# Optimization experiments

Measured on AMD Instinct MI355X. Metric: run time of the kernel, lower is better.

## Reference

```python
import jax, jax.numpy as jnp
import numpy as np
from functools import partial

LEAK = 1.0 / 3.0   # scn default leakiness 0.333
EPS = 1e-4         # scn BatchNormalization default eps


def linkey(c, S):
    return (c[..., 0] * S + c[..., 1]) * S + c[..., 2]


def sub_offsets(K):
    r = K // 2
    g = np.stack(np.meshgrid(*([np.arange(-r, r + 1)] * 3), indexing='ij'), -1).reshape(-1, 3)
    return jnp.asarray(g, jnp.int32)


def down_offsets(s):
    g = np.stack(np.meshgrid(*([np.arange(s)] * 3), indexing='ij'), -1).reshape(-1, 3)
    return jnp.asarray(g, jnp.int32)


@partial(jax.checkpoint, static_argnums=(4, 5))
def sparse_conv(out_coords, in_coords, in_feats, W, S_in, stride, offsets):
    """Rulebook gather-GEMM-scatter via sorted-key binary search.
    out_coords [M,3], in_coords [N,3] sorted by linearized key, in_feats [N,Cin],
    W [K3,Cin,Cout]. Submanifold: stride=1, centered offsets, out_coords==in_coords.
    Strided scn.Convolution: offsets 0..stride-1, out sites = unique(in//stride)."""
    in_keys = linkey(in_coords, S_in)  # sorted [N]
    Nin = in_keys.shape[0]

    def body(acc, kw):
        off, Wk = kw
        child = out_coords * stride + off                       # [M,3]
        valid = jnp.all((child >= 0) & (child < S_in), axis=-1)
        nkey = linkey(child, S_in)
        idx = jnp.searchsorted(in_keys, nkey)
        idxc = jnp.clip(idx, 0, Nin - 1)
        found = valid & (in_keys[idxc] == nkey)
        g = jnp.where(found[:, None], in_feats[idxc], 0.0)      # gather, zero for inactive
        return acc + g @ Wk, None

    acc0 = jnp.zeros((out_coords.shape[0], W.shape[-1]), in_feats.dtype)
    acc, _ = jax.lax.scan(body, acc0, (offsets, W))
    return acc


def bn_lrelu(x, g, b):
    m = x.mean(0)
    v = x.var(0)
    y = (x - m) * (g / jnp.sqrt(v + EPS)) + b
    return jnp.where(y > 0, y, LEAK * y)


def lrelu(x):
    return jnp.where(x > 0, x, LEAK * x)


def forward_core(floats, c0, c1, c2, c3, c4):
    (feats0, W_init, Wd1, gd1, bd1, W11a, g11, b11, W11b,
     W12a, g12, b12, W12b, Wd2, gd2, bd2,
     W21a, g21, b21, W21b, W22a, g22, b22, W22b,
     Wd3, gd3, bd3, Wd4, gd4, bd4, W2, b2, W3, b3) = floats
    o3 = sub_offsets(3)
    x = sparse_conv(c0, c0, feats0, W_init, 512, 1, sub_offsets(7))                 # [N0,64] @512
    x = bn_lrelu(sparse_conv(c1, c0, x, Wd1, 512, 2, down_offsets(2)), gd1, bd1)    # [N1,64] @256
    res = x
    h = bn_lrelu(sparse_conv(c1, c1, x, W11a, 256, 1, o3), g11, b11)
    x = lrelu(sparse_conv(c1, c1, h, W11b, 256, 1, o3) + res)
    res = x
    h = bn_lrelu(sparse_conv(c1, c1, x, W12a, 256, 1, o3), g12, b12)
    x = lrelu(sparse_conv(c1, c1, h, W12b, 256, 1, o3) + res)
    x = bn_lrelu(sparse_conv(c2, c1, x, Wd2, 256, 2, down_offsets(2)), gd2, bd2)    # [N2,128] @128
    res = x
    h = bn_lrelu(sparse_conv(c2, c2, x, W21a, 128, 1, o3), g21, b21)
    x = lrelu(sparse_conv(c2, c2, h, W21b, 128, 1, o3) + res)
    res = x
    h = bn_lrelu(sparse_conv(c2, c2, x, W22a, 128, 1, o3), g22, b22)
    x = lrelu(sparse_conv(c2, c2, h, W22b, 128, 1, o3) + res)
    x = bn_lrelu(sparse_conv(c3, c2, x, Wd3, 128, 4, down_offsets(4)), gd3, bd3)    # [N3,64] @32
    x = bn_lrelu(sparse_conv(c4, c3, x, Wd4, 32, 4, down_offsets(4)), gd4, bd4)     # [N4,2]  @8
    # SparseToDense -> dense [2,8,8,8], then torch .view(-1, 2*8*8*8) (channel-major)
    k4 = linkey(c4, 8)
    dense = jnp.zeros((8 * 8 * 8, 2), x.dtype).at[k4].set(x)    # [512,2]
    flat = dense.T.reshape(1, -1)                               # [1,1024]
    v = jax.nn.elu(flat @ W2 + b2)
    return jax.nn.sigmoid(v @ W3 + b3)                          # [1,1]


def _decode(k, S):
    a = k // (S * S)
    r = k % (S * S)
    return np.stack([a, r // S, r % S], -1).astype(np.int32)


def setup_inputs() -> dict:
    rng = np.random.default_rng(0)
    N0 = 50000
    k0 = np.unique(rng.integers(0, 512 ** 3, size=N0 + 20000))[:N0]
    c0 = _decode(k0, 512)
    c1 = _decode(np.unique((c0[:, 0].astype(np.int64) // 2 * 256 + c0[:, 1] // 2) * 256 + c0[:, 2] // 2), 256)
    c2 = _decode(np.unique((c1[:, 0].astype(np.int64) // 2 * 128 + c1[:, 1] // 2) * 128 + c1[:, 2] // 2), 128)
    c3 = _decode(np.unique((c2[:, 0].astype(np.int64) // 4 * 32 + c2[:, 1] // 4) * 32 + c2[:, 2] // 4), 32)
    c4 = _decode(np.unique((c3[:, 0].astype(np.int64) // 4 * 8 + c3[:, 1] // 4) * 8 + c3[:, 2] // 4), 8)
    key = jax.random.key(0)
    ks = jax.random.split(key, 20)

    def w(i, shape, fan):
        return jax.random.normal(ks[i], shape, jnp.float32) / np.float32(np.sqrt(fan))

    return dict(
        feats0=jax.random.normal(ks[0], (N0, 1), jnp.float32),
        W_init=w(1, (343, 1, 64), 343.0),
        Wd1=w(2, (8, 64, 64), 8 * 64), gd1=jnp.ones(64), bd1=jnp.zeros(64),
        W11a=w(3, (27, 64, 64), 27 * 64), g11=jnp.ones(64), b11=jnp.zeros(64),
        W11b=w(4, (27, 64, 64), 27 * 64),
        W12a=w(5, (27, 64, 64), 27 * 64), g12=jnp.ones(64), b12=jnp.zeros(64),
        W12b=w(6, (27, 64, 64), 27 * 64),
        Wd2=w(7, (8, 64, 128), 8 * 64), gd2=jnp.ones(128), bd2=jnp.zeros(128),
        W21a=w(8, (27, 128, 128), 27 * 128), g21=jnp.ones(128), b21=jnp.zeros(128),
        W21b=w(9, (27, 128, 128), 27 * 128),
        W22a=w(10, (27, 128, 128), 27 * 128), g22=jnp.ones(128), b22=jnp.zeros(128),
        W22b=w(11, (27, 128, 128), 27 * 128),
        Wd3=w(12, (64, 128, 64), 64 * 128), gd3=jnp.ones(64), bd3=jnp.zeros(64),
        Wd4=w(13, (64, 64, 2), 64 * 64), gd4=jnp.ones(2), bd4=jnp.zeros(2),
        W2=w(14, (1024, 2), 1024.0), b2=jnp.zeros(2),
        W3=w(15, (2, 1), 2.0), b3=jnp.zeros(1),
        coords0=jnp.asarray(c0), coords1=jnp.asarray(c1), coords2=jnp.asarray(c2),
        coords3=jnp.asarray(c3), coords4=jnp.asarray(c4),
    )


def reference(feats0, W_init, Wd1, gd1, bd1, W11a, g11, b11, W11b, W12a, g12, b12, W12b,
              Wd2, gd2, bd2, W21a, g21, b21, W21b, W22a, g22, b22, W22b,
              Wd3, gd3, bd3, Wd4, gd4, bd4, W2, b2, W3, b3,
              coords0, coords1, coords2, coords3, coords4):
    floats = (feats0, W_init, Wd1, gd1, bd1, W11a, g11, b11, W11b, W12a, g12, b12, W12b,
              Wd2, gd2, bd2, W21a, g21, b21, W21b, W22a, g22, b22, W22b,
              Wd3, gd3, bd3, Wd4, gd4, bd4, W2, b2, W3, b3)
    return forward_core(floats, coords0, coords1, coords2, coords3, coords4)
```

## Files before the change

kernel.cpp:

```cpp
#include <hip/hip_runtime.h>

#define LEAKF (1.0f/3.0f)
#define BN_EPS 1e-4f

__device__ __forceinline__ unsigned hmix(int key) {
    unsigned h = (unsigned)key * 2654435761u;
    h ^= h >> 15;
    return h;
}

__device__ __forceinline__ int hlookup(const int* __restrict__ hk,
                                       const int* __restrict__ hv,
                                       int mask, int key) {
    unsigned h = hmix(key) & (unsigned)mask;
    while (true) {
        int k = hk[h];
        if (k == key) return hv[h];
        if (k == -1) return -1;
        h = (h + 1) & (unsigned)mask;
    }
}

__device__ __forceinline__ float bnl(float v, float s, float h) {
    v = v * s + h;
    return v > 0.f ? v : v * LEAKF;
}

__global__ __launch_bounds__(256) void build_hash_bm_all(
    int B0, int B1, int B2,
    int N0, const int* __restrict__ c0, int* __restrict__ hk0, int* __restrict__ hv0,
    int m0, unsigned* __restrict__ bm0,
    int N1, const int* __restrict__ c1, int* __restrict__ hk1, int* __restrict__ hv1,
    int m1, unsigned* __restrict__ bm1,
    int N2, const int* __restrict__ c2, int* __restrict__ hk2, int* __restrict__ hv2,
    int m2, unsigned* __restrict__ bm2,
    int N3, const int* __restrict__ c3, int* __restrict__ hk3, int* __restrict__ hv3,
    int m3) {
    const int* coords; int* hk; int* hv; unsigned* bm; int mask, S, N, i;
    int b = blockIdx.x;
    if (b < B0)           { coords = c0; hk = hk0; hv = hv0; bm = bm0; mask = m0; S = 512; N = N0; i = b * 256 + threadIdx.x; }
    else if (b < B0 + B1) { coords = c1; hk = hk1; hv = hv1; bm = bm1; mask = m1; S = 256; N = N1; i = (b - B0) * 256 + threadIdx.x; }
    else if (b < B0 + B1 + B2) { coords = c2; hk = hk2; hv = hv2; bm = bm2; mask = m2; S = 128; N = N2; i = (b - B0 - B1) * 256 + threadIdx.x; }
    else                  { coords = c3; hk = hk3; hv = hv3; bm = nullptr; mask = m3; S = 32; N = N3; i = (b - B0 - B1 - B2) * 256 + threadIdx.x; }
    if (i >= N) return;
    int key = (coords[3 * i] * S + coords[3 * i + 1]) * S + coords[3 * i + 2];
    if (bm) atomicOr(&bm[key >> 5], 1u << (key & 31));
    unsigned h = hmix(key) & (unsigned)mask;
    while (true) {
        int old = atomicCAS(&hk[h], -1, key);
        if (old == -1 || old == key) { hv[h] = i; break; }
        h = (h + 1) & (unsigned)mask;
    }
}

__global__ __launch_bounds__(256) void rb_sub_bm(
    int B1,
    int N1, const int* __restrict__ c1, const unsigned* __restrict__ bm1,
    const int* __restrict__ hk1, const int* __restrict__ hv1, int m1,
    int2* __restrict__ rb1, int* __restrict__ cnt1, int cap1,
    int N2, const int* __restrict__ c2, const unsigned* __restrict__ bm2,
    const int* __restrict__ hk2, const int* __restrict__ hv2, int m2,
    int2* __restrict__ rb2, int* __restrict__ cnt2, int cap2) {
    __shared__ int lcnt[27];
    __shared__ int lbase[27];
    int tid = threadIdx.x;
    if (tid < 27) lcnt[tid] = 0;
    __syncthreads();
    const int* coords; const unsigned* bm; const int* hk; const int* hv;
    int mask, S, N, t; int2* pairs; int* counts; int cap;
    if (blockIdx.x < B1) {
        coords = c1; bm = bm1; hk = hk1; hv = hv1; mask = m1; S = 256; N = N1;
        pairs = rb1; counts = cnt1; cap = cap1; t = blockIdx.x * 256 + tid;
    } else {
        coords = c2; bm = bm2; hk = hk2; hv = hv2; mask = m2; S = 128; N = N2;
        pairs = rb2; counts = cnt2; cap = cap2; t = (blockIdx.x - B1) * 256 + tid;
    }
    unsigned bits = 0;
    int m = 0, kmin = 0, z = 0, dx = 0, dy = 0;
    int rk[3], ix[3];
    if (t < N * 9) {
        m = t / 9;
        int od = t - m * 9;
        dx = od / 3 - 1;
        dy = od - (od / 3) * 3 - 1;
        int x = coords[3 * m] + dx;
        int y = coords[3 * m + 1] + dy;
        z = coords[3 * m + 2];
        if ((unsigned)x < (unsigned)S && (unsigned)y < (unsigned)S) {
            int zmin = z - 1 < 0 ? 0 : z - 1;
            int zmax = z + 1 > S - 1 ? S - 1 : z + 1;
            kmin = (x * S + y) * S + zmin;
            int wi = kmin >> 5, sh = kmin & 31, nb = zmax - zmin + 1;
            unsigned long long w =
                ((unsigned long long)bm[wi + 1] << 32) | (unsigned long long)bm[wi];
            bits = (unsigned)((w >> sh) & ((1u << nb) - 1u));
            if (dx == 0 && dy == 0) bits &= ~(1u << (z - zmin));
            unsigned tmp = bits;
            int nf = 0;
            while (tmp) {
                int bb = __ffs(tmp) - 1;
                tmp &= tmp - 1;
                ix[nf] = hlookup(hk, hv, mask, kmin + bb);
                int dz = (kmin & (S - 1)) + bb - z;
                int k = (dx + 1) * 9 + (dy + 1) * 3 + (dz + 1);
                rk[nf] = atomicAdd(&lcnt[k], 1);
                nf++;
            }
        }
    }
    __syncthreads();
    if (tid < 27 && lcnt[tid] > 0) lbase[tid] = atomicAdd(&counts[tid], lcnt[tid]);
    __syncthreads();
    {
        unsigned tmp = bits;
        int j = 0;
        while (tmp) {
            int bb = __ffs(tmp) - 1;
            tmp &= tmp - 1;
            int dz = (kmin & (S - 1)) + bb - z;
            int k = (dx + 1) * 9 + (dy + 1) * 3 + (dz + 1);
            int p = lbase[k] + rk[j];
            if (p < cap) pairs[(size_t)k * cap + p] = make_int2(m, ix[j]);
            j++;
        }
    }
}

__global__ __launch_bounds__(256) void rb_down_all(
    int B1, int B2,
    int N0, const int* __restrict__ c0, const int* __restrict__ hk1,
    const int* __restrict__ hv1, int m1, int2* __restrict__ rbD1,
    int* __restrict__ cntD1, int capD1,
    int N1, const int* __restrict__ c1, const int* __restrict__ hk2,
    const int* __restrict__ hv2, int m2, int2* __restrict__ rbD2,
    int* __restrict__ cntD2, int capD2,
    int N2, const int* __restrict__ c2, const int* __restrict__ hk3,
    const int* __restrict__ hv3, int m3, int2* __restrict__ rbD3,
    int* __restrict__ cntD3, int capD3) {
    __shared__ int lcnt[64];
    __shared__ int lbase[64];
    int tid = threadIdx.x;
    const int* cin; const int* hk; const int* hv;
    int mask, Sout, s, Nin, i; int2* pairs; int* counts; int cap;
    int b = blockIdx.x;
    if (b < B1) {
        cin = c0; hk = hk1; hv = hv1; mask = m1; Sout = 256; s = 2; Nin = N0;
        pairs = rbD1; counts = cntD1; cap = capD1; i = b * 256 + tid;
    } else if (b < B1 + B2) {
        cin = c1; hk = hk2; hv = hv2; mask = m2; Sout = 128; s = 2; Nin = N1;
        pairs = rbD2; counts = cntD2; cap = capD2; i = (b - B1) * 256 + tid;
    } else {
        cin = c2; hk = hk3; hv = hv3; mask = m3; Sout = 32; s = 4; Nin = N2;
        pairs = rbD3; counts = cntD3; cap = capD3; i = (b - B1 - B2) * 256 + tid;
    }
    int K3 = s * s * s;
    if (tid < K3) lcnt[tid] = 0;
    __syncthreads();
    int k = -1, m = -1, rank = 0;
    if (i < Nin) {
        int x = cin[3 * i], y = cin[3 * i + 1], z = cin[3 * i + 2];
        k = ((x % s) * s + (y % s)) * s + (z % s);
        int key = ((x / s) * Sout + (y / s)) * Sout + (z / s);
        m = hlookup(hk, hv, mask, key);
        rank = atomicAdd(&lcnt[k], 1);
    }
    __syncthreads();
    if (tid < K3 && lcnt[tid] > 0) lbase[tid] = atomicAdd(&counts[tid], lcnt[tid]);
    __syncthreads();
    if (i < Nin) {
        int p = lbase[k] + rank;
        if (p < cap) pairs[(size_t)k * cap + p] = make_int2(m, i);
    }
}

__global__ __launch_bounds__(256) void init_probe(
    int total, int chunk, const int* __restrict__ c0, const unsigned* __restrict__ bm,
    const int* __restrict__ hk, const int* __restrict__ hv, int mask,
    int2* __restrict__ pairs, int* __restrict__ pcount, int cap) {
    __shared__ int lcnt, lbase;
    int tid = threadIdx.x;
    if (tid == 0) lcnt = 0;
    __syncthreads();
    int b = blockIdx.x;
    int nb = (b & 7) * chunk + (b >> 3);
    int t = nb * 256 + tid;
    unsigned bits = 0;
    int m = -1, kmin = 0, z = 0, dx = 0, dy = 0, rank = 0;
    if (t < total) {
        m = t / 49;
        int od = t - m * 49;
        dx = od / 7 - 3;
        dy = od - (od / 7) * 7 - 3;
        int x = c0[3 * m] + dx;
        int y = c0[3 * m + 1] + dy;
        z = c0[3 * m + 2];
        if ((unsigned)x < 512u && (unsigned)y < 512u) {
            int zmin = z - 3 < 0 ? 0 : z - 3;
            int zmax = z + 3 > 511 ? 511 : z + 3;
            kmin = (x * 512 + y) * 512 + zmin;
            int wi = kmin >> 5, sh = kmin & 31, nb2 = zmax - zmin + 1;
            unsigned long long w =
                ((unsigned long long)bm[wi + 1] << 32) | (unsigned long long)bm[wi];
            bits = (unsigned)((w >> sh) & ((1u << nb2) - 1u));
            if (dx == 0 && dy == 0) bits &= ~(1u << (z - zmin));
            if (bits) rank = atomicAdd(&lcnt, __popc(bits));
        }
    }
    __syncthreads();
    if (tid == 0 && lcnt > 0) lbase = atomicAdd(pcount, lcnt);
    __syncthreads();
    while (bits) {
        int b2 = __ffs(bits) - 1;
        bits &= bits - 1;
        int nkey = kmin + b2;
        int idx = hlookup(hk, hv, mask, nkey);
        int dz = (kmin & 511) + b2 - z;
        int k = (dx + 3) * 49 + (dy + 3) * 7 + (dz + 3);
        int p = lbase + rank++;
        if (p < cap) pairs[p] = make_int2(m, idx | (k << 17));
    }
}

__global__ __launch_bounds__(256) void init_center(
    int N0, const float* __restrict__ f0, const float* __restrict__ W,
    float* __restrict__ out) {
    int t = blockIdx.x * 256 + threadIdx.x;
    if (t >= N0 * 64) return;
    int m = t >> 6, co = t & 63;
    out[t] = f0[m] * W[171 * 64 + co];
}

__global__ __launch_bounds__(256) void init_apply(
    const int2* __restrict__ pairs, const int* __restrict__ pcount, int cap,
    const float* __restrict__ f0, const float* __restrict__ W,
    float* __restrict__ out) {
    int P = min(*pcount, cap);
    int t = blockIdx.x * 256 + threadIdx.x;
    if (t >= P * 64) return;
    int p = t >> 6, co = t & 63;
    int2 pr = pairs[p];
    int idx = pr.y & 0x1FFFF, k = pr.y >> 17;
    atomicAdd(&out[(size_t)pr.x * 64 + co], f0[idx] * W[k * 64 + co]);
}

template <int C, int TS, bool BNF>
__global__ __launch_bounds__(256) void center_gemm(
    int N, const float* __restrict__ inF, const float* __restrict__ Wc,
    float* __restrict__ out, const float* __restrict__ scp,
    const float* __restrict__ shp) {
    constexpr int C4 = C / 4;
    constexpr int SP = TS / 8;
    __shared__ float sW[C * 64];
    __shared__ float4 sRow[TS * C4];
    int tid = threadIdx.x;
    int t0 = blockIdx.x * TS;
    int co0 = blockIdx.y << 6;
    for (int e = tid; e < C * 16; e += 256) {
        int ci = e >> 4, c4 = e & 15;
        ((float4*)sW)[e] = *(const float4*)(Wc + (size_t)ci * C + co0 + c4 * 4);
    }
    for (int e = tid; e < TS * C4; e += 256) {
        int p = e / C4, c4 = e - p * C4;
        float4 v = make_float4(0.f, 0.f, 0.f, 0.f);
        if (t0 + p < N) {
            v = ((const float4*)inF)[(size_t)(t0 + p) * C4 + c4];
            if (BNF) {
                float4 s4 = ((const float4*)scp)[c4];
                float4 h4 = ((const float4*)shp)[c4];
                v.x = bnl(v.x, s4.x, h4.x);
                v.y = bnl(v.y, s4.y, h4.y);
                v.z = bnl(v.z, s4.z, h4.z);
                v.w = bnl(v.w, s4.w, h4.w);
            }
        }
        sRow[e] = v;
    }
    __syncthreads();
    int co = tid & 31, sg = tid >> 5;
    float accA[SP], accB[SP];
#pragma unroll
    for (int j = 0; j < SP; j++) { accA[j] = 0.f; accB[j] = 0.f; }
    for (int c4 = 0; c4 < C4; c4++) {
        float a0 = sW[(c4 * 4 + 0) * 64 + co];
        float a1 = sW[(c4 * 4 + 1) * 64 + co];
        float a2 = sW[(c4 * 4 + 2) * 64 + co];
        float a3 = sW[(c4 * 4 + 3) * 64 + co];
        float b0 = sW[(c4 * 4 + 0) * 64 + co + 32];
        float b1 = sW[(c4 * 4 + 1) * 64 + co + 32];
        float b2 = sW[(c4 * 4 + 2) * 64 + co + 32];
        float b3 = sW[(c4 * 4 + 3) * 64 + co + 32];
#pragma unroll
        for (int j = 0; j < SP; j++) {
            float4 r = sRow[(sg * SP + j) * C4 + c4];
            accA[j] += r.x * a0 + r.y * a1 + r.z * a2 + r.w * a3;
            accB[j] += r.x * b0 + r.y * b1 + r.z * b2 + r.w * b3;
        }
    }
#pragma unroll
    for (int j = 0; j < SP; j++) {
        int p = sg * SP + j;
        if (t0 + p < N) {
            out[(size_t)(t0 + p) * C + co0 + co] = accA[j];
            out[(size_t)(t0 + p) * C + co0 + co + 32] = accB[j];
        }
    }
}

template <int CIN, int P, int MODE>
__global__ __launch_bounds__(256) void pair_gemm(
    const float* __restrict__ inF, const float* __restrict__ inF2,
    const float* __restrict__ W, float* __restrict__ out,
    const int2* __restrict__ pairs, const int* __restrict__ counts,
    int cap, int chunksPerK, int COUT,
    const float* __restrict__ scp, const float* __restrict__ shp) {
    constexpr int C4 = CIN / 4;
    constexpr int SP = P / 8;
    __shared__ float sW[CIN * 64];
    __shared__ float4 sRow[P * C4];
    __shared__ int sM[P];
    __shared__ int sIdx[P];
    int k = blockIdx.x / chunksPerK;
    int chunk = blockIdx.x - k * chunksPerK;
    int cnt = min(counts[k], cap);
    int base = chunk * P;
    if (base >= cnt) return;
    int Pact = min(P, cnt - base);
    int tid = threadIdx.x;
    if (tid < P) {
        if (tid < Pact) {
            int2 pr = pairs[(size_t)k * cap + base + tid];
            sM[tid] = pr.x;
            sIdx[tid] = pr.y;
        } else {
            sM[tid] = -1;
            sIdx[tid] = 0;
        }
    }
    __syncthreads();
    int co0 = blockIdx.y << 6;
    const float* gW = W + (size_t)k * CIN * COUT + co0;
    for (int e = tid; e < CIN * 16; e += 256) {
        int ci = e >> 4, c4 = e & 15;
        ((float4*)sW)[e] = *(const float4*)(gW + (size_t)ci * COUT + c4 * 4);
    }
    for (int e = tid; e < P * C4; e += 256) {
        int p = e / C4, c4 = e - p * C4;
        float4 v = make_float4(0.f, 0.f, 0.f, 0.f);
        if (p < Pact) {
            v = ((const float4*)inF)[(size_t)sIdx[p] * C4 + c4];
            if (MODE == 1) {
                float4 s4 = ((const float4*)scp)[c4];
                float4 h4 = ((const float4*)shp)[c4];
                v.x = bnl(v.x, s4.x, h4.x);
                v.y = bnl(v.y, s4.y, h4.y);
                v.z = bnl(v.z, s4.z, h4.z);
                v.w = bnl(v.w, s4.w, h4.w);
            } else if (MODE == 2) {
                float4 u = ((const float4*)inF2)[(size_t)sIdx[p] * C4 + c4];
                v.x += u.x; v.y += u.y; v.z += u.z; v.w += u.w;
                v.x = v.x > 0.f ? v.x : v.x * LEAKF;
                v.y = v.y > 0.f ? v.y : v.y * LEAKF;
                v.z = v.z > 0.f ? v.z : v.z * LEAKF;
                v.w = v.w > 0.f ? v.w : v.w * LEAKF;
            }
        }
        sRow[e] = v;
    }
    __syncthreads();
    int co = tid & 31, sg = tid >> 5;
    float accA[SP], accB[SP];
#pragma unroll
    for (int j = 0; j < SP; j++) { accA[j] = 0.f; accB[j] = 0.f; }
    for (int c4 = 0; c4 < C4; c4++) {
        float a0 = sW[(c4 * 4 + 0) * 64 + co];
        float a1 = sW[(c4 * 4 + 1) * 64 + co];
        float a2 = sW[(c4 * 4 + 2) * 64 + co];
        float a3 = sW[(c4 * 4 + 3) * 64 + co];
        float b0 = sW[(c4 * 4 + 0) * 64 + co + 32];
        float b1 = sW[(c4 * 4 + 1) * 64 + co + 32];
        float b2 = sW[(c4 * 4 + 2) * 64 + co + 32];
        float b3 = sW[(c4 * 4 + 3) * 64 + co + 32];
#pragma unroll
        for (int j = 0; j < SP; j++) {
            float4 r = sRow[(sg * SP + j) * C4 + c4];
            accA[j] += r.x * a0 + r.y * a1 + r.z * a2 + r.w * a3;
            accB[j] += r.x * b0 + r.y * b1 + r.z * b2 + r.w * b3;
        }
    }
#pragma unroll
    for (int j = 0; j < SP; j++) {
        int p = sg * SP + j;
        if (p < Pact) {
            atomicAdd(&out[(size_t)sM[p] * COUT + co0 + co], accA[j]);
            atomicAdd(&out[(size_t)sM[p] * COUT + co0 + co + 32], accB[j]);
        }
    }
}

__global__ __launch_bounds__(64) void convd4_kernel(
    int M, const int* __restrict__ oc, const float* __restrict__ x3,
    const float* __restrict__ W, float* __restrict__ out4,
    const int* __restrict__ hk, const int* __restrict__ hv, int mask,
    const float* __restrict__ scp, const float* __restrict__ shp) {
    __shared__ int sIdx[64];
    __shared__ int sK[64];
    __shared__ int sCount;
    int m = blockIdx.x, tid = threadIdx.x;
    int cx = oc[3 * m], cy = oc[3 * m + 1], cz = oc[3 * m + 2];
    if (tid == 0) sCount = 0;
    __syncthreads();
    {
        int k = tid;
        int a = k >> 4, b = (k >> 2) & 3, c = k & 3;
        int x = cx * 4 + a, y = cy * 4 + b, z = cz * 4 + c;
        int key = (x * 32 + y) * 32 + z;
        int idx = hlookup(hk, hv, mask, key);
        if (idx >= 0) { int p = atomicAdd(&sCount, 1); sIdx[p] = idx; sK[p] = k; }
    }
    __syncthreads();
    int cnt = sCount;
    float s = scp[tid], h = shp[tid];
    float a0 = 0.f, a1 = 0.f;
    for (int j = 0; j < cnt; j++) {
        int idx = sIdx[j], k = sK[j];
        float f = bnl(x3[(size_t)idx * 64 + tid], s, h);
        const float* wk = W + ((size_t)k * 64 + tid) * 2;
        a0 += f * wk[0];
        a1 += f * wk[1];
    }
    for (int o = 32; o > 0; o >>= 1) {
        a0 += __shfl_down(a0, o);
        a1 += __shfl_down(a1, o);
    }
    if (tid == 0) { out4[2 * m] = a0; out4[2 * m + 1] = a1; }
}

__global__ __launch_bounds__(256) void bn_reduce_fin(
    const float4* __restrict__ X4, int total4, int B4, int C, int Cmask, float invN,
    const float* __restrict__ g, const float* __restrict__ b,
    float* __restrict__ sums, int* __restrict__ done,
    float* __restrict__ sc, float* __restrict__ sh) {
    __shared__ float sS[128];
    __shared__ float sQ[128];
    __shared__ int isLast;
    int tid = threadIdx.x;
    if (tid < C) { sS[tid] = 0.f; sQ[tid] = 0.f; }
    __syncthreads();
    int base4 = blockIdx.x * B4;
    int end4 = min(base4 + B4, total4);
    float s0 = 0.f, s1 = 0.f, s2 = 0.f, s3 = 0.f;
    float q0 = 0.f, q1 = 0.f, q2 = 0.f, q3 = 0.f;
    for (int e4 = base4 + tid; e4 < end4; e4 += 256) {
        float4 v = X4[e4];
        s0 += v.x; q0 += v.x * v.x;
        s1 += v.y; q1 += v.y * v.y;
        s2 += v.z; q2 += v.z * v.z;
        s3 += v.w; q3 += v.w * v.w;
    }
    int c0 = (4 * (base4 + tid)) & Cmask;
    atomicAdd(&sS[c0], s0);               atomicAdd(&sQ[c0], q0);
    atomicAdd(&sS[(c0 + 1) & Cmask], s1); atomicAdd(&sQ[(c0 + 1) & Cmask], q1);
    atomicAdd(&sS[(c0 + 2) & Cmask], s2); atomicAdd(&sQ[(c0 + 2) & Cmask], q2);
    atomicAdd(&sS[(c0 + 3) & Cmask], s3); atomicAdd(&sQ[(c0 + 3) & Cmask], q3);
    __syncthreads();
    if (tid < C) {
        atomicAdd(&sums[tid], sS[tid]);
        atomicAdd(&sums[128 + tid], sQ[tid]);
    }
    __syncthreads();
    if (tid == 0) {
        __threadfence();
        int t = atomicAdd(done, 1);
        isLast = (t == (int)gridDim.x - 1);
    }
    __syncthreads();
    if (isLast) {
        if (tid < C) {
            float v1 = atomicAdd(&sums[tid], 0.0f);
            float v2 = atomicAdd(&sums[128 + tid], 0.0f);
            float mean = v1 * invN;
            float var = v2 * invN - mean * mean;
            float s = g[tid] / sqrtf(var + BN_EPS);
            sc[tid] = s;
            sh[tid] = b[tid] - mean * s;
            sums[tid] = 0.f;
            sums[128 + tid] = 0.f;
        }
        if (tid == 0) *done = 0;
    }
}

__global__ __launch_bounds__(256) void add_lrelu_bn(const float4* __restrict__ A,
                                                    const float4* __restrict__ X,
                                                    float4* __restrict__ Y, int total4,
                                                    int C4mask,
                                                    const float* __restrict__ scp,
                                                    const float* __restrict__ shp) {
    int e = blockIdx.x * 256 + threadIdx.x;
    if (e >= total4) return;
    int c4 = e & C4mask;
    float4 s4 = ((const float4*)scp)[c4];
    float4 h4 = ((const float4*)shp)[c4];
    float4 a = A[e], x = X[e], v;
    v.x = a.x + bnl(x.x, s4.x, h4.x);
    v.y = a.y + bnl(x.y, s4.y, h4.y);
    v.z = a.z + bnl(x.z, s4.z, h4.z);
    v.w = a.w + bnl(x.w, s4.w, h4.w);
    v.x = v.x > 0.f ? v.x : v.x * LEAKF;
    v.y = v.y > 0.f ? v.y : v.y * LEAKF;
    v.z = v.z > 0.f ? v.z : v.z * LEAKF;
    v.w = v.w > 0.f ? v.w : v.w * LEAKF;
    Y[e] = v;
}

__global__ __launch_bounds__(256) void bn_scatter(int M, const int* __restrict__ c4,
                                                  const float* __restrict__ x4,
                                                  const float* __restrict__ sc,
                                                  const float* __restrict__ sh,
                                                  float* __restrict__ dense) {
    int i = blockIdx.x * 256 + threadIdx.x;
    if (i >= 2 * M) return;
    int m = i >> 1, co = i & 1;
    float v = x4[i] * sc[co] + sh[co];
    v = v > 0.f ? v : v * LEAKF;
    int key = (c4[3 * m] * 8 + c4[3 * m + 1]) * 8 + c4[3 * m + 2];
    dense[key * 2 + co] = v;
}

__global__ __launch_bounds__(256) void head_kernel(const float* __restrict__ dense,
                                                   const float* __restrict__ W2,
                                                   const float* __restrict__ b2,
                                                   const float* __restrict__ W3,
                                                   const float* __restrict__ b3,
                                                   float* __restrict__ out) {
    __shared__ float r0[256];
    __shared__ float r1[256];
    int tid = threadIdx.x;
    float a0 = 0.f, a1 = 0.f;
    for (int j = tid; j < 1024; j += 256) {
        int co = j >> 9, k = j & 511;
        float f = dense[k * 2 + co];
        a0 += f * W2[2 * j];
        a1 += f * W2[2 * j + 1];
    }
    r0[tid] = a0;
    r1[tid] = a1;
    __syncthreads();
    for (int s = 128; s > 0; s >>= 1) {
        if (tid < s) { r0[tid] += r0[tid + s]; r1[tid] += r1[tid + s]; }
        __syncthreads();
    }
    if (tid == 0) {
        float v0 = r0[0] + b2[0];
        float v1 = r1[0] + b2[1];
        v0 = v0 > 0.f ? v0 : expm1f(v0);
        v1 = v1 > 0.f ? v1 : expm1f(v1);
        float z = v0 * W3[0] + v1 * W3[1] + b3[0];
        out[0] = 1.f / (1.f + expf(-z));
    }
}

extern "C" void kernel_launch(void* const* d_in, const int* in_sizes, int n_in,
                              void* d_out, int out_size, void* d_ws, size_t ws_size,
                              hipStream_t stream) {
    const float* F0    = (const float*)d_in[0];
    const float* Winit = (const float*)d_in[1];
    const float* Wd1   = (const float*)d_in[2];
    const float* gd1   = (const float*)d_in[3];
    const float* bd1   = (const float*)d_in[4];
    const float* W11a  = (const float*)d_in[5];
    const float* g11   = (const float*)d_in[6];
    const float* b11   = (const float*)d_in[7];
    const float* W11b  = (const float*)d_in[8];
    const float* W12a  = (const float*)d_in[9];
    const float* g12   = (const float*)d_in[10];
    const float* b12   = (const float*)d_in[11];
    const float* W12b  = (const float*)d_in[12];
    const float* Wd2   = (const float*)d_in[13];
    const float* gd2   = (const float*)d_in[14];
    const float* bd2   = (const float*)d_in[15];
    const float* W21a  = (const float*)d_in[16];
    const float* g21   = (const float*)d_in[17];
    const float* b21   = (const float*)d_in[18];
    const float* W21b  = (const float*)d_in[19];
    const float* W22a  = (const float*)d_in[20];
    const float* g22   = (const float*)d_in[21];
    const float* b22   = (const float*)d_in[22];
    const float* W22b  = (const float*)d_in[23];
    const float* Wd3   = (const float*)d_in[24];
    const float* gd3   = (const float*)d_in[25];
    const float* bd3   = (const float*)d_in[26];
    const float* Wd4   = (const float*)d_in[27];
    const float* gd4   = (const float*)d_in[28];
    const float* bd4   = (const float*)d_in[29];
    const float* W2    = (const float*)d_in[30];
    const float* b2    = (const float*)d_in[31];
    const float* W3    = (const float*)d_in[32];
    const float* b3    = (const float*)d_in[33];
    const int* c0 = (const int*)d_in[34];
    const int* c1 = (const int*)d_in[35];
    const int* c2 = (const int*)d_in[36];
    const int* c3 = (const int*)d_in[37];
    const int* c4 = (const int*)d_in[38];
    int N0 = in_sizes[34] / 3, N1 = in_sizes[35] / 3, N2 = in_sizes[36] / 3;
    int N3 = in_sizes[37] / 3, N4 = in_sizes[38] / 3;

    char* base = (char*)d_ws;
    size_t off = 0;
    auto alloc = [&](size_t bytes) -> void* {
        void* p = base + off;
        off = (off + bytes + 255) & ~(size_t)255;
        return p;
    };
    const int CAP0 = 262144, CAP = 131072, CAP3 = 65536;
    size_t hs_off = off;
    int* hk0 = (int*)alloc((size_t)CAP0 * 4);
    int* hv0 = (int*)alloc((size_t)CAP0 * 4);
    int* hk1 = (int*)alloc((size_t)CAP * 4);
    int* hv1 = (int*)alloc((size_t)CAP * 4);
    int* hk2 = (int*)alloc((size_t)CAP * 4);
    int* hv2 = (int*)alloc((size_t)CAP * 4);
    int* hk3 = (int*)alloc((size_t)CAP3 * 4);
    int* hv3 = (int*)alloc((size_t)CAP3 * 4);
    size_t he_off = off;
    size_t zs_off = off;
    float* sums = (float*)alloc(256 * 4);
    float* scb = (float*)alloc(8 * 128 * 4);
    float* shb = (float*)alloc(8 * 128 * 4);
    float* dense = (float*)alloc(1024 * 4);
    float* x4 = (float*)alloc(1032 * 4);
    int* counts = (int*)alloc(136 * 4);
    unsigned* bm1 = (unsigned*)alloc((size_t)(524288 + 2) * 4);
    unsigned* bm2 = (unsigned*)alloc((size_t)(65536 + 2) * 4);
    size_t ze_off = off;
    int* cntS1 = counts, *cntS2 = counts + 27, *cntD1 = counts + 54, *cntD2 = counts + 62,
       * cntD3 = counts + 70;
    int* done = counts + 134;
    int* pcount = counts + 135;
    const int CAP_S1 = 1024, CAP_S2 = 4096, CAP_D1 = 8192, CAP_D2 = 8192, CAP_D3 = 1024;
    const int CAPP = 16384;
    int2* pairs0 = (int2*)alloc((size_t)CAPP * 8);
    int2* rbS1 = (int2*)alloc((size_t)27 * CAP_S1 * 8);
    int2* rbS2 = (int2*)alloc((size_t)27 * CAP_S2 * 8);
    int2* rbD1 = (int2*)alloc((size_t)8 * CAP_D1 * 8);
    int2* rbD2 = (int2*)alloc((size_t)8 * CAP_D2 * 8);
    int2* rbD3 = (int2*)alloc((size_t)64 * CAP_D3 * 8);
    size_t relems = (size_t)N0 * 64;
    if ((size_t)N2 * 128 > relems) relems = (size_t)N2 * 128;
    float* R1 = (float*)alloc(relems * 4);
    float* R2 = (float*)alloc(relems * 4);
    float* R3 = (float*)alloc(relems * 4);
    unsigned* bm0 = (unsigned*)R1;

    hipMemsetAsync(base + hs_off, 0xFF, he_off - hs_off, stream);
    hipMemsetAsync(base + zs_off, 0x00, ze_off - zs_off, stream);
    hipMemsetAsync(bm0, 0x00, (size_t)(1 << 24) + 64, stream);

    int Bh0 = (N0 + 255) / 256, Bh1 = (N1 + 255) / 256, Bh2 = (N2 + 255) / 256,
        Bh3 = (N3 + 255) / 256;
    build_hash_bm_all<<<Bh0 + Bh1 + Bh2 + Bh3, 256, 0, stream>>>(
        Bh0, Bh1, Bh2,
        N0, c0, hk0, hv0, CAP0 - 1, bm0,
        N1, c1, hk1, hv1, CAP - 1, bm1,
        N2, c2, hk2, hv2, CAP - 1, bm2,
        N3, c3, hk3, hv3, CAP3 - 1);
    int Bs1 = (N1 * 9 + 255) / 256, Bs2 = (N2 * 9 + 255) / 256;
    rb_sub_bm<<<Bs1 + Bs2, 256, 0, stream>>>(
        Bs1,
        N1, c1, bm1, hk1, hv1, CAP - 1, rbS1, cntS1, CAP_S1,
        N2, c2, bm2, hk2, hv2, CAP - 1, rbS2, cntS2, CAP_S2);
    rb_down_all<<<Bh0 + Bh1 + Bh2, 256, 0, stream>>>(
        Bh0, Bh1,
        N0, c0, hk1, hv1, CAP - 1, rbD1, cntD1, CAP_D1,
        N1, c1, hk2, hv2, CAP - 1, rbD2, cntD2, CAP_D2,
        N2, c2, hk3, hv3, CAP3 - 1, rbD3, cntD3, CAP_D3);

    auto bnstats = [&](const float* X, int N, int C, const float* g, const float* b,
                       int slot) {
        int total4 = (N * C + 3) >> 2;
        int B4 = 32 * C;
        int grid = (total4 + B4 - 1) / B4;
        bn_reduce_fin<<<grid, 256, 0, stream>>>((const float4*)X, total4, B4, C, C - 1,
                                                1.0f / (float)N, g, b, sums, done,
                                                scb + slot * 128, shb + slot * 128);
    };
    const int CH_S1 = CAP_S1 / 128;
    const int CH_S2 = (CAP_S2 + 79) / 80;
    auto sub64 = [&](const float* X, const float* W, float* Y, int slot) {
        if (slot >= 0) {
            center_gemm<64, 128, true><<<dim3((N1 + 127) / 128, 1), 256, 0, stream>>>(
                N1, X, W + 13 * 64 * 64, Y, scb + slot * 128, shb + slot * 128);
            pair_gemm<64, 128, 1><<<dim3(27 * CH_S1, 1), 256, 0, stream>>>(
                X, nullptr, W, Y, rbS1, cntS1, CAP_S1, CH_S1, 64,
                scb + slot * 128, shb + slot * 128);
        } else {
            center_gemm<64, 128, false><<<dim3((N1 + 127) / 128, 1), 256, 0, stream>>>(
                N1, X, W + 13 * 64 * 64, Y, nullptr, nullptr);
            pair_gemm<64, 128, 0><<<dim3(27 * CH_S1, 1), 256, 0, stream>>>(
                X, nullptr, W, Y, rbS1, cntS1, CAP_S1, CH_S1, 64, nullptr, nullptr);
        }
    };
    auto sub128 = [&](const float* X, const float* W, float* Y, int slot) {
        if (slot >= 0) {
            center_gemm<128, 80, true><<<dim3((N2 + 79) / 80, 2), 256, 0, stream>>>(
                N2, X, W + 13 * 128 * 128, Y, scb + slot * 128, shb + slot * 128);
            pair_gemm<128, 80, 1><<<dim3(27 * CH_S2, 2), 256, 0, stream>>>(
                X, nullptr, W, Y, rbS2, cntS2, CAP_S2, CH_S2, 128,
                scb + slot * 128, shb + slot * 128);
        } else {
            center_gemm<128, 80, false><<<dim3((N2 + 79) / 80, 2), 256, 0, stream>>>(
                N2, X, W + 13 * 128 * 128, Y, nullptr, nullptr);
            pair_gemm<128, 80, 0><<<dim3(27 * CH_S2, 2), 256, 0, stream>>>(
                X, nullptr, W, Y, rbS2, cntS2, CAP_S2, CH_S2, 128, nullptr, nullptr);
        }
    };

    int totProbe = N0 * 49;
    int Gp = (totProbe + 255) / 256;
    int chunkP = (Gp + 7) / 8;
    init_probe<<<8 * chunkP, 256, 0, stream>>>(totProbe, chunkP, c0, bm0,
                                               hk0, hv0, CAP0 - 1, pairs0, pcount, CAPP);
    init_center<<<(N0 * 64 + 255) / 256, 256, 0, stream>>>(N0, F0, Winit, R3);
    init_apply<<<(CAPP * 64) / 256, 256, 0, stream>>>(pairs0, pcount, CAPP, F0, Winit, R3);

    hipMemsetAsync(R1, 0, (size_t)N1 * 64 * 4, stream);
    pair_gemm<64, 128, 0><<<dim3(8 * (CAP_D1 / 128), 1), 256, 0, stream>>>(
        R3, nullptr, Wd1, R1, rbD1, cntD1, CAP_D1, CAP_D1 / 128, 64, nullptr, nullptr);
    bnstats(R1, N1, 64, gd1, bd1, 0);

    sub64(R1, W11a, R2, 0);
    bnstats(R2, N1, 64, g11, b11, 1);
    sub64(R2, W11b, R3, 1);
    add_lrelu_bn<<<(N1 * 16 + 255) / 256, 256, 0, stream>>>(
        (const float4*)R3, (const float4*)R1, (float4*)R2, N1 * 16, 15, scb, shb);
    sub64(R2, W12a, R3, -1);
    bnstats(R3, N1, 64, g12, b12, 2);
    sub64(R3, W12b, R1, 2);

    hipMemsetAsync(R3, 0, (size_t)N2 * 128 * 4, stream);
    pair_gemm<64, 128, 2><<<dim3(8 * (CAP_D2 / 128), 2), 256, 0, stream>>>(
        R1, R2, Wd2, R3, rbD2, cntD2, CAP_D2, CAP_D2 / 128, 128, nullptr, nullptr);
    bnstats(R3, N2, 128, gd2, bd2, 3);

    sub128(R3, W21a, R1, 3);
    bnstats(R1, N2, 128, g21, b21, 4);
    sub128(R1, W21b, R2, 4);
    add_lrelu_bn<<<(N2 * 32 + 255) / 256, 256, 0, stream>>>(
        (const float4*)R2, (const float4*)R3, (float4*)R1, N2 * 32, 31,
        scb + 3 * 128, shb + 3 * 128);
    sub128(R1, W22a, R2, -1);
    bnstats(R2, N2, 128, g22, b22, 5);
    sub128(R2, W22b, R3, 5);

    hipMemsetAsync(R2, 0, (size_t)N3 * 64 * 4, stream);
    {
        const int CH3 = (CAP_D3 + 79) / 80;
        pair_gemm<128, 80, 2><<<dim3(64 * CH3, 1), 256, 0, stream>>>(
            R3, R1, Wd3, R2, rbD3, cntD3, CAP_D3, CH3, 64, nullptr, nullptr);
    }
    bnstats(R2, N3, 64, gd3, bd3, 6);

    convd4_kernel<<<N4, 64, 0, stream>>>(N4, c4, R2, Wd4, x4, hk3, hv3, CAP3 - 1,
                                         scb + 6 * 128, shb + 6 * 128);
    bnstats(x4, N4, 2, gd4, bd4, 7);
    bn_scatter<<<(2 * N4 + 255) / 256, 256, 0, stream>>>(N4, c4, x4, scb + 7 * 128,
                                                         shb + 7 * 128, dense);

    head_kernel<<<1, 256, 0, stream>>>(dense, W2, b2, W3, b3, (float*)d_out);
}
```

Baseline: 1.134 ms.

## Shrink pair/center GEMM tiles and interleave block-to-offset mapping across XCDs

```diff
diff --git a/kernel.cpp b/kernel.cpp
--- a/kernel.cpp
+++ b/kernel.cpp
@@ -311,7 +311,7 @@
     const float* __restrict__ inF, const float* __restrict__ inF2,
     const float* __restrict__ W, float* __restrict__ out,
     const int2* __restrict__ pairs, const int* __restrict__ counts,
-    int cap, int chunksPerK, int COUT,
+    int cap, int chunksPerK, int totalNb, int COUT,
     const float* __restrict__ scp, const float* __restrict__ shp) {
     constexpr int C4 = CIN / 4;
     constexpr int SP = P / 8;
@@ -319,8 +319,11 @@
     __shared__ float4 sRow[P * C4];
     __shared__ int sM[P];
     __shared__ int sIdx[P];
-    int k = blockIdx.x / chunksPerK;
-    int chunk = blockIdx.x - k * chunksPerK;
+    int b = blockIdx.x;
+    int nb = (b & 7) * (gridDim.x >> 3) + (b >> 3);
+    if (nb >= totalNb) return;
+    int k = nb / chunksPerK;
+    int chunk = nb - k * chunksPerK;
     int cnt = min(counts[k], cap);
     int base = chunk * P;
     if (base >= cnt) return;
@@ -684,34 +687,38 @@
                                                 1.0f / (float)N, g, b, sums, done,
                                                 scb + slot * 128, shb + slot * 128);
     };
-    const int CH_S1 = CAP_S1 / 128;
-    const int CH_S2 = (CAP_S2 + 79) / 80;
+    const int CH_S1 = CAP_S1 / 64;
+    const int CH_S2 = CAP_S2 / 32;
+    const int CH_D12 = CAP_D1 / 64;
+    const int CH_D3 = CAP_D3 / 32;
     auto sub64 = [&](const float* X, const float* W, float* Y, int slot) {
         if (slot >= 0) {
-            center_gemm<64, 128, true><<<dim3((N1 + 127) / 128, 1), 256, 0, stream>>>(
+            center_gemm<64, 64, true><<<dim3((N1 + 63) / 64, 1), 256, 0, stream>>>(
                 N1, X, W + 13 * 64 * 64, Y, scb + slot * 128, shb + slot * 128);
-            pair_gemm<64, 128, 1><<<dim3(27 * CH_S1, 1), 256, 0, stream>>>(
-                X, nullptr, W, Y, rbS1, cntS1, CAP_S1, CH_S1, 64,
+            pair_gemm<64, 64, 1><<<dim3(27 * CH_S1, 1), 256, 0, stream>>>(
+                X, nullptr, W, Y, rbS1, cntS1, CAP_S1, CH_S1, 27 * CH_S1, 64,
                 scb + slot * 128, shb + slot * 128);
         } else {
-            center_gemm<64, 128, false><<<dim3((N1 + 127) / 128, 1), 256, 0, stream>>>(
+            center_gemm<64, 64, false><<<dim3((N1 + 63) / 64, 1), 256, 0, stream>>>(
                 N1, X, W + 13 * 64 * 64, Y, nullptr, nullptr);
-            pair_gemm<64, 128, 0><<<dim3(27 * CH_S1, 1), 256, 0, stream>>>(
-                X, nullptr, W, Y, rbS1, cntS1, CAP_S1, CH_S1, 64, nullptr, nullptr);
+            pair_gemm<64, 64, 0><<<dim3(27 * CH_S1, 1), 256, 0, stream>>>(
+                X, nullptr, W, Y, rbS1, cntS1, CAP_S1, CH_S1, 27 * CH_S1, 64,
+                nullptr, nullptr);
         }
     };
     auto sub128 = [&](const float* X, const float* W, float* Y, int slot) {
         if (slot >= 0) {
-            center_gemm<128, 80, true><<<dim3((N2 + 79) / 80, 2), 256, 0, stream>>>(
+            center_gemm<128, 48, true><<<dim3((N2 + 47) / 48, 2), 256, 0, stream>>>(
                 N2, X, W + 13 * 128 * 128, Y, scb + slot * 128, shb + slot * 128);
-            pair_gemm<128, 80, 1><<<dim3(27 * CH_S2, 2), 256, 0, stream>>>(
-                X, nullptr, W, Y, rbS2, cntS2, CAP_S2, CH_S2, 128,
+            pair_gemm<128, 32, 1><<<dim3(27 * CH_S2, 2), 256, 0, stream>>>(
+                X, nullptr, W, Y, rbS2, cntS2, CAP_S2, CH_S2, 27 * CH_S2, 128,
                 scb + slot * 128, shb + slot * 128);
         } else {
-            center_gemm<128, 80, false><<<dim3((N2 + 79) / 80, 2), 256, 0, stream>>>(
+            center_gemm<128, 48, false><<<dim3((N2 + 47) / 48, 2), 256, 0, stream>>>(
                 N2, X, W + 13 * 128 * 128, Y, nullptr, nullptr);
-            pair_gemm<128, 80, 0><<<dim3(27 * CH_S2, 2), 256, 0, stream>>>(
-                X, nullptr, W, Y, rbS2, cntS2, CAP_S2, CH_S2, 128, nullptr, nullptr);
+            pair_gemm<128, 32, 0><<<dim3(27 * CH_S2, 2), 256, 0, stream>>>(
+                X, nullptr, W, Y, rbS2, cntS2, CAP_S2, CH_S2, 27 * CH_S2, 128,
+                nullptr, nullptr);
         }
     };
 
@@ -724,8 +731,9 @@
     init_apply<<<(CAPP * 64) / 256, 256, 0, stream>>>(pairs0, pcount, CAPP, F0, Winit, R3);
 
     hipMemsetAsync(R1, 0, (size_t)N1 * 64 * 4, stream);
-    pair_gemm<64, 128, 0><<<dim3(8 * (CAP_D1 / 128), 1), 256, 0, stream>>>(
-        R3, nullptr, Wd1, R1, rbD1, cntD1, CAP_D1, CAP_D1 / 128, 64, nullptr, nullptr);
+    pair_gemm<64, 64, 0><<<dim3(8 * CH_D12, 1), 256, 0, stream>>>(
+        R3, nullptr, Wd1, R1, rbD1, cntD1, CAP_D1, CH_D12, 8 * CH_D12, 64,
+        nullptr, nullptr);
     bnstats(R1, N1, 64, gd1, bd1, 0);
 
     sub64(R1, W11a, R2, 0);
@@ -738,8 +746,9 @@
     sub64(R3, W12b, R1, 2);
 
     hipMemsetAsync(R3, 0, (size_t)N2 * 128 * 4, stream);
-    pair_gemm<64, 128, 2><<<dim3(8 * (CAP_D2 / 128), 2), 256, 0, stream>>>(
-        R1, R2, Wd2, R3, rbD2, cntD2, CAP_D2, CAP_D2 / 128, 128, nullptr, nullptr);
+    pair_gemm<64, 64, 2><<<dim3(8 * CH_D12, 2), 256, 0, stream>>>(
+        R1, R2, Wd2, R3, rbD2, cntD2, CAP_D2, CH_D12, 8 * CH_D12, 128,
+        nullptr, nullptr);
     bnstats(R3, N2, 128, gd2, bd2, 3);
 
     sub128(R3, W21a, R1, 3);
@@ -753,11 +762,9 @@
     sub128(R2, W22b, R3, 5);
 
     hipMemsetAsync(R2, 0, (size_t)N3 * 64 * 4, stream);
-    {
-        const int CH3 = (CAP_D3 + 79) / 80;
-        pair_gemm<128, 80, 2><<<dim3(64 * CH3, 1), 256, 0, stream>>>(
-            R3, R1, Wd3, R2, rbD3, cntD3, CAP_D3, CH3, 64, nullptr, nullptr);
-    }
+    pair_gemm<128, 32, 2><<<dim3(64 * CH_D3, 1), 256, 0, stream>>>(
+        R3, R1, Wd3, R2, rbD3, cntD3, CAP_D3, CH_D3, 64 * CH_D3, 64,
+        nullptr, nullptr);
     bnstats(R2, N3, 64, gd3, bd3, 6);
 
     convd4_kernel<<<N4, 64, 0, stream>>>(N4, c4, R2, Wd4, x4, hk3, hv3, CAP3 - 1,
```

Result: faster. 1.101 ms (-2.9%).
